# Performance work log

Measured on AMD Instinct MI355X. Metric: run time of the kernel, lower is better.

Reference implementation:

```python
import jax, jax.numpy as jnp
import numpy as np

NUM_FEATURES = 81   # atom feature width used in matmuls
N_NODES = 262144
N_COLS = 103        # num_features + num_bond
OUT_CH = 128
COORD = 3           # distance rule slice [0:3]


def setup_inputs() -> dict:
    key = jax.random.key(0)
    k1, k2, k3, k4 = jax.random.split(key, 4)
    features = jax.random.normal(k1, (N_NODES, N_COLS), dtype=jnp.float32)
    # columns 81, 82 hold neighbor indices (0 => no neighbor), stored as floats
    idx = jax.random.randint(k4, (N_NODES, 2), 0, N_NODES).astype(jnp.float32)
    features = features.at[:, NUM_FEATURES:NUM_FEATURES + 2].set(idx)
    w_s = jax.random.normal(k2, (NUM_FEATURES, OUT_CH), dtype=jnp.float32) * 0.05
    w_n = jax.random.normal(k3, (N_COLS, OUT_CH), dtype=jnp.float32) * 0.05
    return {"features": features, "w_s": w_s, "w_n": w_n}


def reference(features, w_s, w_n):
    F = NUM_FEATURES
    self_f = features[:, :F]                       # [N, F]
    new_features = self_f @ w_s                    # [N, C] self term

    idx0 = features[:, F].astype(jnp.int32)        # neighbor slot 0
    idx1 = features[:, F + 1].astype(jnp.int32)    # neighbor slot 1

    def neighbor_contrib(idx):
        nei = features[idx]                                        # gather [N, 103]
        # rule 0: 'distance' over [0:COORD] -> keep neighbor slice, record distance
        d = jnp.sqrt(jnp.sum(jnp.square(self_f[:, :COORD] - nei[:, :COORD]), axis=-1))
        seg_dist = nei[:, :COORD]                                  # [N, 3]
        # rule 1: 'sum' over [COORD:F]
        seg_sum = self_f[:, COORD:F] + nei[:, COORD:F]             # [N, F-3]
        comb = jnp.concatenate([seg_dist, seg_sum], axis=-1)       # [N, F]
        d_eff = jnp.where(d > 0, d, jnp.float32(0.01))
        comb = comb / jnp.square(d_eff)[:, None]                   # distance scaling
        return comb @ w_n[:F] + new_features                       # tiny-matmul batched

    c0 = neighbor_contrib(idx0)
    c1 = neighbor_contrib(idx1)
    # rows with no valid neighbor were never written -> zeros
    out = jnp.where((idx1 != 0)[:, None], c1,
                    jnp.where((idx0 != 0)[:, None], c0, jnp.float32(0.0)))
    return out
```

## Files before the change

kernel.cpp:

```cpp
#include <hip/hip_runtime.h>
#include <hip/hip_bf16.h>

constexpr int kNodes = 262144;
constexpr int NC  = 103;
constexpr int F   = 81;
constexpr int OC  = 128;
constexpr int NKS = 6;
constexpr int NPB = 64;
constexpr int THREADS = 256;
constexpr int NEI_STRIDE = 101;
constexpr int GW = 96;

typedef __attribute__((ext_vector_type(8))) short bf16x8;
typedef __attribute__((ext_vector_type(4))) float f32x4;

__device__ inline ushort f2bf(float f) {
  uint u = __float_as_uint(f);
  return (ushort)((u + 0x7fffu + ((u >> 16) & 1u)) >> 16);
}
__device__ inline short bfc(float x) {
  return (short)__bfloat16_as_ushort(__float2bfloat16(x));
}

__global__ __launch_bounds__(256)
void prep_w(const float* __restrict__ w_s, const float* __restrict__ w_n,
            ushort* __restrict__ wf) {
  int t = blockIdx.x * 256 + threadIdx.x;
  if (t >= NKS * 8 * 64) return;
  int l  = t & 63;
  int ct = (t >> 6) & 7;
  int ks = t >> 9;
  int c  = ct * 16 + (l & 15);
  int kb = ks * 32 + ((l >> 4) << 3);
  union { ushort u[8]; int4 v; } o;
  #pragma unroll
  for (int i = 0; i < 8; ++i) {
    int k = kb + i;
    float f = 0.f;
    if (k < F)                      f = w_s[k * OC + c];
    else if (k >= 96 && k < 96 + F) f = w_n[(k - 96) * OC + c];
    o.u[i] = f2bf(f);
  }
  ((int4*)wf)[t] = o.v;
}

__global__ __launch_bounds__(THREADS)
void rgc_v12(const float* __restrict__ feat, const ushort* __restrict__ wf,
             float* __restrict__ out) {
  __shared__ __align__(16) float lds_self[NPB * NC];
  __shared__ __align__(16) float lds_nei[NPB * NEI_STRIDE];
  __shared__ int   s_sel[NPB];
  __shared__ float s_cs[NPB];

  const int tid = threadIdx.x;
  const int w   = tid >> 6;
  const int l   = tid & 63;
  const long base = (long)blockIdx.x * NPB;
  const float* fbase = feat + base * NC;

  const bf16x8* wfv = (const bf16x8*)wf;
  bf16x8 bA[NKS], bB[NKS];
  #pragma unroll
  for (int ks = 0; ks < NKS; ++ks) {
    bA[ks] = wfv[(ks * 8 + w)     * 64 + l];
    bB[ks] = wfv[(ks * 8 + w + 4) * 64 + l];
  }

  if (l < 16) {
    const int n = w * 16 + l;
    const float* row = feat + (base + n) * NC;
    float f0 = row[F], f1 = row[F + 1];
    int i0 = (int)f0, i1 = (int)f1;
    int sel = (i1 != 0) ? i1 : i0;
    const float* nr = feat + (long)sel * NC;
    float dx = row[0] - nr[0];
    float dy = row[1] - nr[1];
    float dz = row[2] - nr[2];
    float d2 = dx * dx + dy * dy + dz * dz;
    float alive = (sel != 0) ? 1.f : 0.f;
    s_sel[n] = sel;
    s_cs[n]  = alive * ((d2 > 0.f) ? (1.f / d2) : 10000.f);
  }

  {
    const float4* src = (const float4*)fbase;
    float4* dst = (float4*)lds_self;
    #pragma unroll
    for (int i = tid; i < NPB * NC / 4; i += THREADS) dst[i] = src[i];
  }
  __syncthreads();

  #pragma unroll
  for (int j = 0; j < 24; ++j) {
    int v   = tid + j * THREADS;
    int row = v / GW;
    int col = v - row * GW;
    lds_nei[row * NEI_STRIDE + col] = feat[(long)s_sel[row] * NC + col];
  }
  __syncthreads();

  const int q    = l >> 4;
  const int lrow = l & 15;
  const int off0 = q * 8;
  const int col  = l & 15;

  #pragma unroll
  for (int nt = 0; nt < 4; ++nt) {
    const int n = nt * 16 + lrow;
    const float* sp = lds_self + n * NC;
    const float* np = lds_nei + n * NEI_STRIDE;
    const float alive = (s_sel[n] != 0) ? 1.f : 0.f;
    const float cs    = s_cs[n];

    bf16x8 afS[3], afC[3];
    #pragma unroll
    for (int c = 0; c < 3; ++c) {
      #pragma unroll
      for (int i = 0; i < 8; ++i) {
        float sv = sp[c * 32 + off0 + i];
        float nv = np[c * 32 + off0 + i];
        afS[c][i] = bfc(sv * alive);
        float se = sv;
        if (c == 0 && i < 3 && q == 0) se = 0.f;
        afC[c][i] = bfc((nv + se) * cs);
      }
    }

    f32x4 a0 = (f32x4)(0.f), a1 = (f32x4)(0.f);
    #pragma unroll
    for (int ks = 0; ks < NKS; ++ks) {
      bf16x8 af = (ks < 3) ? afS[ks] : afC[ks - 3];
      a0 = __builtin_amdgcn_mfma_f32_16x16x32_bf16(af, bA[ks], a0, 0, 0, 0);
      a1 = __builtin_amdgcn_mfma_f32_16x16x32_bf16(af, bB[ks], a1, 0, 0, 0);
    }

    const long orow = base + nt * 16 + q * 4;
    #pragma unroll
    for (int r = 0; r < 4; ++r) {
      out[(orow + r) * OC + w * 16       + col] = a0[r];
      out[(orow + r) * OC + (w + 4) * 16 + col] = a1[r];
    }
  }
}

extern "C" void kernel_launch(void* const* d_in, const int* in_sizes, int n_in,
                              void* d_out, int out_size, void* d_ws, size_t ws_size,
                              hipStream_t stream) {
  const float* feat = (const float*)d_in[0];
  const float* w_s  = (const float*)d_in[1];
  const float* w_n  = (const float*)d_in[2];
  float* outp = (float*)d_out;
  ushort* wf = (ushort*)d_ws;

  prep_w<<<dim3((NKS * 8 * 64 + 255) / 256), 256, 0, stream>>>(w_s, w_n, wf);
  rgc_v12<<<dim3(kNodes / NPB), THREADS, 0, stream>>>(feat, wf, outp);
}
```

Measured before the change: 75.11 us.

## Load self and neighbor rows directly into LDS with swizzled layout

Replaces the register-staged copies of the self tile and the gathered neighbor rows with global_load_lds direct-to-LDS loads. Neighbor rows are stored with an XOR swizzle so the MMA operand build can read them with 16-byte vector LDS loads without bank conflicts. The distance computation moves after the gather and reads from LDS, which removes the extra dependent global loads of the neighbor coordinates. In exchange the code relies on raw barriers and waitcnt asm, and the swizzle indexing has to be exactly right for correctness.

```diff
diff --git a/kernel.cpp b/kernel.cpp
--- a/kernel.cpp
+++ b/kernel.cpp
@@ -8,8 +8,8 @@
 constexpr int NKS = 6;
 constexpr int NPB = 64;
 constexpr int THREADS = 256;
-constexpr int NEI_STRIDE = 101;
-constexpr int GW = 96;
+constexpr int NST = 96;
+constexpr int SELF_F4 = NPB * NC / 4;
 
 typedef __attribute__((ext_vector_type(8))) short bf16x8;
 typedef __attribute__((ext_vector_type(4))) float f32x4;
@@ -20,6 +20,17 @@
 }
 __device__ inline short bfc(float x) {
   return (short)__bfloat16_as_ushort(__float2bfloat16(x));
+}
+
+__device__ __forceinline__ void gll4(const float* g, float* l) {
+  __builtin_amdgcn_global_load_lds(
+      (const __attribute__((address_space(1))) unsigned int*)g,
+      (__attribute__((address_space(3))) unsigned int*)l, 4, 0, 0);
+}
+__device__ __forceinline__ void gll16(const float* g, float* l) {
+  __builtin_amdgcn_global_load_lds(
+      (const __attribute__((address_space(1))) unsigned int*)g,
+      (__attribute__((address_space(3))) unsigned int*)l, 16, 0, 0);
 }
 
 __global__ __launch_bounds__(256)
@@ -45,10 +56,10 @@
 }
 
 __global__ __launch_bounds__(THREADS)
-void rgc_v12(const float* __restrict__ feat, const ushort* __restrict__ wf,
+void rgc_v13(const float* __restrict__ feat, const ushort* __restrict__ wf,
              float* __restrict__ out) {
   __shared__ __align__(16) float lds_self[NPB * NC];
-  __shared__ __align__(16) float lds_nei[NPB * NEI_STRIDE];
+  __shared__ __align__(16) float lds_nei[NPB * NST];
   __shared__ int   s_sel[NPB];
   __shared__ float s_cs[NPB];
 
@@ -66,38 +77,54 @@
     bB[ks] = wfv[(ks * 8 + w + 4) * 64 + l];
   }
 
+  #pragma unroll
+  for (int j = 0; j < 7; ++j) {
+    int i = tid + j * THREADS;
+    if (j < 6 || i < SELF_F4) {
+      gll16((const float*)((const float4*)fbase + i),
+            (float*)((float4*)lds_self + (j * THREADS + w * 64)));
+    }
+  }
   if (l < 16) {
     const int n = w * 16 + l;
     const float* row = feat + (base + n) * NC;
     float f0 = row[F], f1 = row[F + 1];
     int i0 = (int)f0, i1 = (int)f1;
-    int sel = (i1 != 0) ? i1 : i0;
-    const float* nr = feat + (long)sel * NC;
-    float dx = row[0] - nr[0];
-    float dy = row[1] - nr[1];
-    float dz = row[2] - nr[2];
-    float d2 = dx * dx + dy * dy + dz * dz;
-    float alive = (sel != 0) ? 1.f : 0.f;
-    s_sel[n] = sel;
-    s_cs[n]  = alive * ((d2 > 0.f) ? (1.f / d2) : 10000.f);
+    s_sel[n] = (i1 != 0) ? i1 : i0;
   }
-
-  {
-    const float4* src = (const float4*)fbase;
-    float4* dst = (float4*)lds_self;
-    #pragma unroll
-    for (int i = tid; i < NPB * NC / 4; i += THREADS) dst[i] = src[i];
-  }
-  __syncthreads();
+  asm volatile("s_waitcnt lgkmcnt(0)" ::: "memory");
+  __builtin_amdgcn_s_barrier();
 
   #pragma unroll
   for (int j = 0; j < 24; ++j) {
     int v   = tid + j * THREADS;
-    int row = v / GW;
-    int col = v - row * GW;
-    lds_nei[row * NEI_STRIDE + col] = feat[(long)s_sel[row] * NC + col];
+    int row = v / NST;
+    int p   = v - row * NST;
+    int c   = p >> 5;
+    int x   = (p >> 2) & 7;
+    int cl  = p & 3;
+    int col = (c << 5) + ((x ^ (row & 7)) << 2) + cl;
+    gll4(feat + (long)s_sel[row] * NC + col,
+         lds_nei + (j * THREADS + w * 64));
   }
-  __syncthreads();
+  asm volatile("s_waitcnt vmcnt(0) lgkmcnt(0)" ::: "memory");
+  __builtin_amdgcn_s_barrier();
+
+  if (tid < NPB) {
+    const int n = tid;
+    const int r = n & 7;
+    float nx = lds_nei[n * NST + r * 4 + 0];
+    float ny = lds_nei[n * NST + r * 4 + 1];
+    float nz = lds_nei[n * NST + r * 4 + 2];
+    float dx = lds_self[n * NC + 0] - nx;
+    float dy = lds_self[n * NC + 1] - ny;
+    float dz = lds_self[n * NC + 2] - nz;
+    float d2 = dx * dx + dy * dy + dz * dz;
+    float alive = (s_sel[n] != 0) ? 1.f : 0.f;
+    s_cs[n] = alive * ((d2 > 0.f) ? (1.f / d2) : 10000.f);
+  }
+  asm volatile("s_waitcnt lgkmcnt(0)" ::: "memory");
+  __builtin_amdgcn_s_barrier();
 
   const int q    = l >> 4;
   const int lrow = l & 15;
@@ -107,18 +134,21 @@
   #pragma unroll
   for (int nt = 0; nt < 4; ++nt) {
     const int n = nt * 16 + lrow;
+    const int r = n & 7;
     const float* sp = lds_self + n * NC;
-    const float* np = lds_nei + n * NEI_STRIDE;
+    const float* np = lds_nei + n * NST;
     const float alive = (s_sel[n] != 0) ? 1.f : 0.f;
     const float cs    = s_cs[n];
 
     bf16x8 afS[3], afC[3];
     #pragma unroll
     for (int c = 0; c < 3; ++c) {
+      f32x4 lo = *(const f32x4*)(np + c * 32 + (((2 * q)     ^ r) << 2));
+      f32x4 hi = *(const f32x4*)(np + c * 32 + (((2 * q + 1) ^ r) << 2));
       #pragma unroll
       for (int i = 0; i < 8; ++i) {
         float sv = sp[c * 32 + off0 + i];
-        float nv = np[c * 32 + off0 + i];
+        float nv = (i < 4) ? lo[i] : hi[i - 4];
         afS[c][i] = bfc(sv * alive);
         float se = sv;
         if (c == 0 && i < 3 && q == 0) se = 0.f;
@@ -136,9 +166,9 @@
 
     const long orow = base + nt * 16 + q * 4;
     #pragma unroll
-    for (int r = 0; r < 4; ++r) {
-      out[(orow + r) * OC + w * 16       + col] = a0[r];
-      out[(orow + r) * OC + (w + 4) * 16 + col] = a1[r];
+    for (int rr = 0; rr < 4; ++rr) {
+      out[(orow + rr) * OC + w * 16       + col] = a0[rr];
+      out[(orow + rr) * OC + (w + 4) * 16 + col] = a1[rr];
     }
   }
 }
@@ -153,5 +183,5 @@
   ushort* wf = (ushort*)d_ws;
 
   prep_w<<<dim3((NKS * 8 * 64 + 255) / 256), 256, 0, stream>>>(w_s, w_n, wf);
-  rgc_v12<<<dim3(kNodes / NPB), THREADS, 0, stream>>>(feat, wf, outp);
+  rgc_v13<<<dim3(kNodes / NPB), THREADS, 0, stream>>>(feat, wf, outp);
 }
```

After: 67.75 us. -9.8%, faster.
